# Optimization experiments

Measured on AMD Instinct MI355X. Metric: run time of the kernel, lower is better.

The kernel has to match this reference:

```python
import jax, jax.numpy as jnp
import numpy as np

DROPOUT_P = 0.2


def setup_inputs() -> dict:
    key = jax.random.key(0)
    kq, kk, kv = jax.random.split(key, 3)
    B, Sq, Sk, D, Dv = 4, 4096, 4096, 64, 64
    return {
        "query": jax.random.normal(kq, (B, Sq, D), dtype=jnp.float32),
        "key": jax.random.normal(kk, (B, Sk, D), dtype=jnp.float32),
        "value": jax.random.normal(kv, (B, Sk, Dv), dtype=jnp.float32),
        "inv_scale_factor": 8,
    }


def reference(query, key, value, inv_scale_factor):
    # qk = Q K^T / inv_scale_factor  -> [B, Sq, Sk]
    scaled_qk = jnp.einsum("bqd,bkd->bqk", query, key) / inv_scale_factor
    probs = jax.nn.softmax(scaled_qk, axis=-1)
    # dropout (train mode, p=0.2) with a fixed key for determinism
    keep = jax.random.bernoulli(jax.random.key(42), 1.0 - DROPOUT_P, probs.shape)
    probs = jnp.where(keep, probs / (1.0 - DROPOUT_P), 0.0)
    # [B, Sq, Sk] @ [B, Sk, Dv] -> [B, Sq, Dv]
    return jnp.einsum("bqk,bkv->bqv", probs, value)
```

## Files before the change

### kernel.cpp

```cpp
#include <hip/hip_runtime.h>
#include <stdint.h>

#define S_LEN 4096
#define D_DIM 64
#define KBLK  64
#define QBLK  64
#define NBATCH 4
#define ROWSTRIDE 66

typedef __attribute__((ext_vector_type(8))) short bf16x8;
typedef __attribute__((ext_vector_type(4))) float f32x4;

#define LOG2E 1.4426950408889634f

__device__ __forceinline__ uint32_t pk_bf16(float lo, float hi) {
    uint32_t r;
    asm("v_cvt_pk_bf16_f32 %0, %1, %2" : "=v"(r) : "v"(lo), "v"(hi));
    return r;
}
__device__ __forceinline__ uint32_t rotl32(uint32_t x, int n) {
    return __builtin_amdgcn_alignbit(x, x, 32 - n);
}

__device__ __forceinline__ uint32_t threefry_xor(uint32_t idx) {
    const uint32_t k0 = 0u, k1 = 42u;
    const uint32_t k2 = 0x1BD11BDAu ^ k0 ^ k1;
    uint32_t x0 = k0;
    uint32_t x1 = idx + k1;
#define TFR(r) { x0 += x1; x1 = rotl32(x1, (r)); x1 ^= x0; }
    TFR(13) TFR(15) TFR(26) TFR(6)
    x0 += k1; x1 += k2 + 1u;
    TFR(17) TFR(29) TFR(16) TFR(24)
    x0 += k2; x1 += k0 + 2u;
    TFR(13) TFR(15) TFR(26) TFR(6)
    x0 += k0; x1 += k1 + 3u;
    TFR(17) TFR(29) TFR(16) TFR(24)
    x0 += k1; x1 += k2 + 4u;
    TFR(13) TFR(15) TFR(26) TFR(6)
    x0 += k2; x1 += k0 + 5u;
#undef TFR
    return x0 ^ x1;
}

#define KEEP_THRESH 0xCCCCCE00u

__device__ __forceinline__ int swzV(int d) {
    return (((d & 7) ^ ((d >> 2) & 7)) << 4);
}

template <bool DIRECT>
__global__ __launch_bounds__(256, 2)
void attn_fwd_kernel(const float* __restrict__ Qp,
                     const float* __restrict__ Kp,
                     const float* __restrict__ Vp,
                     const int* __restrict__ isf,
                     float* __restrict__ outp,
                     int seg_tiles) {
    const int tid  = threadIdx.x;
    const int w    = tid >> 6;
    const int lane = tid & 63;
    const int g    = lane >> 4;
    const int lq   = lane & 15;
    const int b    = blockIdx.y;
    const int qwave = blockIdx.x * QBLK + w * 16;

    __shared__ __align__(16) unsigned char smem[16384];
    unsigned char* Kl = smem;
    unsigned char* Vt = smem + 8192;
    unsigned char* Pl = smem + w * 2048;

    float fv;
    {
        int iv = isf[0];
        if (iv >= 1 && iv <= (1 << 20)) fv = (float)iv;
        else {
            float f = __int_as_float(iv);
            fv = (f > 1.0e-3f && f < 1.0e6f) ? f : 8.0f;
        }
    }
    const float sc = LOG2E / fv;

    bf16x8 qf[2];
    {
        const float* qp = Qp + (size_t)(b * S_LEN + qwave + lq) * D_DIM + 8 * g;
        #pragma unroll
        for (int h = 0; h < 2; ++h) {
            float4 a = *(const float4*)(qp + 32 * h);
            float4 c = *(const float4*)(qp + 32 * h + 4);
            uint32_t w0 = pk_bf16(a.x * sc, a.y * sc);
            uint32_t w1 = pk_bf16(a.z * sc, a.w * sc);
            uint32_t w2 = pk_bf16(c.x * sc, c.y * sc);
            uint32_t w3 = pk_bf16(c.z * sc, c.w * sc);
            bf16x8 f;
            f[0] = (short)(w0 & 0xFFFF); f[1] = (short)(w0 >> 16);
            f[2] = (short)(w1 & 0xFFFF); f[3] = (short)(w1 >> 16);
            f[4] = (short)(w2 & 0xFFFF); f[5] = (short)(w2 >> 16);
            f[6] = (short)(w3 & 0xFFFF); f[7] = (short)(w3 >> 16);
            qf[h] = f;
        }
    }

    f32x4 acc[4];
    #pragma unroll
    for (int nt = 0; nt < 4; ++nt) { acc[nt][0]=0.f; acc[nt][1]=0.f; acc[nt][2]=0.f; acc[nt][3]=0.f; }
    float lrun = 0.0f;

    const float* Kb = Kp + (size_t)b * S_LEN * D_DIM;
    const float* Vb = Vp + (size_t)b * S_LEN * D_DIM;

    const int kt0 = blockIdx.z * seg_tiles;
    for (int kt = kt0; kt < kt0 + seg_tiles; ++kt) {
        const int kbase = kt * KBLK;
        __syncthreads();

        #pragma unroll
        for (int i = 0; i < 4; ++i) {
            int p4 = i * 256 + tid;
            int r  = p4 >> 4, c4 = p4 & 15;
            float4 v = *(const float4*)(Kb + (size_t)(kbase + r) * D_DIM + c4 * 4);
            uint2 wv; wv.x = pk_bf16(v.x, v.y); wv.y = pk_bf16(v.z, v.w);
            *(uint2*)(Kl + ((r * 128 + c4 * 8) ^ ((r & 7) << 4))) = wv;
        }
        #pragma unroll
        for (int i = 0; i < 2; ++i) {
            int pp = i * 256 + tid;
            int kp = pp >> 4, d4 = (pp & 15) * 4;
            const float* vp = Vb + (size_t)(kbase + 2 * kp) * D_DIM + d4;
            float4 a = *(const float4*)vp;
            float4 c = *(const float4*)(vp + D_DIM);
            *(uint32_t*)(Vt + (((d4 + 0) * 128 + kp * 4) ^ swzV(d4 + 0))) = pk_bf16(a.x, c.x);
            *(uint32_t*)(Vt + (((d4 + 1) * 128 + kp * 4) ^ swzV(d4 + 1))) = pk_bf16(a.y, c.y);
            *(uint32_t*)(Vt + (((d4 + 2) * 128 + kp * 4) ^ swzV(d4 + 2))) = pk_bf16(a.z, c.z);
            *(uint32_t*)(Vt + (((d4 + 3) * 128 + kp * 4) ^ swzV(d4 + 3))) = pk_bf16(a.w, c.w);
        }
        __syncthreads();

        f32x4 s[4];
        #pragma unroll
        for (int mt = 0; mt < 4; ++mt) { s[mt][0]=0.f; s[mt][1]=0.f; s[mt][2]=0.f; s[mt][3]=0.f; }
        #pragma unroll
        for (int h = 0; h < 2; ++h) {
            #pragma unroll
            for (int mt = 0; mt < 4; ++mt) {
                int r = 16 * mt + lq;
                bf16x8 kf = *(const bf16x8*)(Kl + ((r * 128 + (4 * h + g) * 16) ^ ((r & 7) << 4)));
                s[mt] = __builtin_amdgcn_mfma_f32_16x16x32_bf16(kf, qf[h], s[mt], 0, 0, 0);
            }
        }
        __syncthreads();

        float pvv[4][4];
        float tsum = 0.f;
        #pragma unroll
        for (int mt = 0; mt < 4; ++mt)
            #pragma unroll
            for (int r = 0; r < 4; ++r) {
                float e = __builtin_amdgcn_exp2f(s[mt][r]);
                pvv[mt][r] = e; tsum += e;
            }
        tsum += __shfl_xor(tsum, 16);
        tsum += __shfl_xor(tsum, 32);
        lrun += tsum;

        const uint32_t base2 = ((uint32_t)b << 24) + ((uint32_t)(qwave + lq) << 12)
                             + (uint32_t)kbase + 4u * (uint32_t)g;
        uint32_t bits[16];
        #pragma unroll
        for (int mt = 0; mt < 4; ++mt)
            #pragma unroll
            for (int r = 0; r < 4; ++r)
                bits[4 * mt + r] = threefry_xor(base2 + (uint32_t)(16 * mt + r));

        #pragma unroll
        for (int mt = 0; mt < 4; ++mt) {
            float pd0 = (bits[4 * mt + 0] < KEEP_THRESH) ? pvv[mt][0] : 0.0f;
            float pd1 = (bits[4 * mt + 1] < KEEP_THRESH) ? pvv[mt][1] : 0.0f;
            float pd2 = (bits[4 * mt + 2] < KEEP_THRESH) ? pvv[mt][2] : 0.0f;
            float pd3 = (bits[4 * mt + 3] < KEEP_THRESH) ? pvv[mt][3] : 0.0f;
            uint2 pw; pw.x = pk_bf16(pd0, pd1); pw.y = pk_bf16(pd2, pd3);
            *(uint2*)(Pl + ((lq * 128 + (16 * mt + 4 * g) * 2) ^ ((lq & 7) << 4))) = pw;
        }

        asm volatile("" ::: "memory");

        #pragma unroll
        for (int kk = 0; kk < 2; ++kk) {
            bf16x8 pf = *(const bf16x8*)(Pl + ((lq * 128 + kk * 64 + g * 16) ^ ((lq & 7) << 4)));
            #pragma unroll
            for (int nt = 0; nt < 4; ++nt) {
                int d = lq + 16 * nt;
                bf16x8 vf = *(const bf16x8*)(Vt + ((d * 128 + kk * 64 + g * 16) ^ swzV(d)));
                acc[nt] = __builtin_amdgcn_mfma_f32_16x16x32_bf16(pf, vf, acc[nt], 0, 0, 0);
            }
        }
    }

    if (DIRECT) {
        float l0 = __shfl(lrun, 4 * g + 0);
        float l1 = __shfl(lrun, 4 * g + 1);
        float l2 = __shfl(lrun, 4 * g + 2);
        float l3 = __shfl(lrun, 4 * g + 3);
        float inv0 = 1.0f / (l0 * 0.8f);
        float inv1 = 1.0f / (l1 * 0.8f);
        float inv2 = 1.0f / (l2 * 0.8f);
        float inv3 = 1.0f / (l3 * 0.8f);
        float* Ob = outp + (size_t)b * S_LEN * D_DIM;
        #pragma unroll
        for (int nt = 0; nt < 4; ++nt) {
            int d = lq + 16 * nt;
            Ob[(size_t)(qwave + 4 * g + 0) * D_DIM + d] = acc[nt][0] * inv0;
            Ob[(size_t)(qwave + 4 * g + 1) * D_DIM + d] = acc[nt][1] * inv1;
            Ob[(size_t)(qwave + 4 * g + 2) * D_DIM + d] = acc[nt][2] * inv2;
            Ob[(size_t)(qwave + 4 * g + 3) * D_DIM + d] = acc[nt][3] * inv3;
        }
    } else {
        float* seg = outp + (size_t)blockIdx.z * NBATCH * S_LEN * ROWSTRIDE;
        size_t row0 = (size_t)b * S_LEN + qwave;
        if (g == 0) {
            float* p = seg + (row0 + lq) * ROWSTRIDE;
            p[0] = 0.0f; p[1] = lrun;
        }
        #pragma unroll
        for (int nt = 0; nt < 4; ++nt) {
            int d = lq + 16 * nt;
            seg[(row0 + 4 * g + 0) * ROWSTRIDE + 2 + d] = acc[nt][0];
            seg[(row0 + 4 * g + 1) * ROWSTRIDE + 2 + d] = acc[nt][1];
            seg[(row0 + 4 * g + 2) * ROWSTRIDE + 2 + d] = acc[nt][2];
            seg[(row0 + 4 * g + 3) * ROWSTRIDE + 2 + d] = acc[nt][3];
        }
    }
}

__global__ void combine_kernel(const float* __restrict__ ws, float* __restrict__ Op, int NS) {
    const int tid = threadIdx.x;
    const size_t row = (size_t)blockIdx.x * 4 + (tid >> 6);
    const int d = tid & 63;
    const size_t SEGF = (size_t)NBATCH * S_LEN * ROWSTRIDE;
    const size_t roff = row * ROWSTRIDE;

    float l = 0.f, o = 0.f;
    for (int s = 0; s < NS; ++s) {
        const float* p = ws + s * SEGF + roff;
        l += p[1];
        o += p[2 + d];
    }
    Op[row * D_DIM + d] = o / (l * 0.8f);
}

extern "C" void kernel_launch(void* const* d_in, const int* in_sizes, int n_in,
                              void* d_out, int out_size, void* d_ws, size_t ws_size,
                              hipStream_t stream) {
    const float* Q = (const float*)d_in[0];
    const float* K = (const float*)d_in[1];
    const float* V = (const float*)d_in[2];
    const int* isf = (const int*)d_in[3];
    float* O = (float*)d_out;

    const size_t SEGB = (size_t)NBATCH * S_LEN * ROWSTRIDE * sizeof(float);
    int NS = 8;
    while (NS > 1 && ws_size < (size_t)NS * SEGB) NS >>= 1;

    if (NS >= 2) {
        dim3 grid1(S_LEN / QBLK, NBATCH, NS);
        attn_fwd_kernel<false><<<grid1, dim3(256), 0, stream>>>(
            Q, K, V, isf, (float*)d_ws, (S_LEN / KBLK) / NS);
        dim3 grid2((NBATCH * S_LEN) / 4);
        combine_kernel<<<grid2, dim3(256), 0, stream>>>((const float*)d_ws, O, NS);
    } else {
        dim3 grid(S_LEN / QBLK, NBATCH, 1);
        attn_fwd_kernel<true><<<grid, dim3(256), 0, stream>>>(
            Q, K, V, isf, O, S_LEN / KBLK);
    }
}
```

Before: 151.8 us.

## Pre-convert K/V to swizzled bf16 and load tiles via global_load_lds

```diff
diff --git a/kernel.cpp b/kernel.cpp
--- a/kernel.cpp
+++ b/kernel.cpp
@@ -7,6 +7,7 @@
 #define QBLK  64
 #define NBATCH 4
 #define ROWSTRIDE 66
+#define PRE_BYTES (2u * 2097152u)
 
 typedef __attribute__((ext_vector_type(8))) short bf16x8;
 typedef __attribute__((ext_vector_type(4))) float f32x4;
@@ -48,14 +49,44 @@
     return (((d & 7) ^ ((d >> 2) & 7)) << 4);
 }
 
+__device__ __forceinline__ void gll16(const void* g, void* l) {
+    __builtin_amdgcn_global_load_lds(
+        (const __attribute__((address_space(1))) uint32_t*)g,
+        (__attribute__((address_space(3))) uint32_t*)l, 16, 0, 0);
+}
+
+__global__ void prep_kernel(const float* __restrict__ Kp,
+                            const float* __restrict__ Vp,
+                            uint32_t* __restrict__ Kpre,
+                            uint32_t* __restrict__ Vpre) {
+    int gid = blockIdx.x * 256 + threadIdx.x;
+    int chunk = gid >> 11;
+    int o = (gid & 2047) << 2;
+    int b = chunk >> 6;
+    int kbase = (chunk & 63) << 6;
+    {
+        int r = o >> 7;
+        int inner = (o & 127) ^ ((r & 7) << 4);
+        int c0 = inner >> 1;
+        const float* src = Kp + ((size_t)b * S_LEN + kbase + r) * D_DIM + c0;
+        Kpre[gid] = pk_bf16(src[0], src[1]);
+    }
+    {
+        int d = o >> 7;
+        int inner = (o & 127) ^ swzV(d);
+        int kp = inner >> 2;
+        const float* src = Vp + ((size_t)b * S_LEN + kbase + 2 * kp) * D_DIM + d;
+        Vpre[gid] = pk_bf16(src[0], src[D_DIM]);
+    }
+}
+
 template <bool DIRECT>
-__global__ __launch_bounds__(256, 2)
-void attn_fwd_kernel(const float* __restrict__ Qp,
-                     const float* __restrict__ Kp,
-                     const float* __restrict__ Vp,
-                     const int* __restrict__ isf,
-                     float* __restrict__ outp,
-                     int seg_tiles) {
+__global__ void attn_fwd_kernel(const float* __restrict__ Qp,
+                                const unsigned char* __restrict__ Kpre,
+                                const unsigned char* __restrict__ Vpre,
+                                const int* __restrict__ isf,
+                                float* __restrict__ outp,
+                                int seg_tiles) {
     const int tid  = threadIdx.x;
     const int w    = tid >> 6;
     const int lane = tid & 63;
@@ -64,10 +95,10 @@
     const int b    = blockIdx.y;
     const int qwave = blockIdx.x * QBLK + w * 16;
 
-    __shared__ __align__(16) unsigned char smem[16384];
+    __shared__ __align__(16) unsigned char smem[24576];
     unsigned char* Kl = smem;
     unsigned char* Vt = smem + 8192;
-    unsigned char* Pl = smem + w * 2048;
+    unsigned char* Pl = smem + 16384 + w * 2048;
 
     float fv;
     {
@@ -105,33 +136,20 @@
     for (int nt = 0; nt < 4; ++nt) { acc[nt][0]=0.f; acc[nt][1]=0.f; acc[nt][2]=0.f; acc[nt][3]=0.f; }
     float lrun = 0.0f;
 
-    const float* Kb = Kp + (size_t)b * S_LEN * D_DIM;
-    const float* Vb = Vp + (size_t)b * S_LEN * D_DIM;
-
     const int kt0 = blockIdx.z * seg_tiles;
     for (int kt = kt0; kt < kt0 + seg_tiles; ++kt) {
         const int kbase = kt * KBLK;
         __syncthreads();
 
-        #pragma unroll
-        for (int i = 0; i < 4; ++i) {
-            int p4 = i * 256 + tid;
-            int r  = p4 >> 4, c4 = p4 & 15;
-            float4 v = *(const float4*)(Kb + (size_t)(kbase + r) * D_DIM + c4 * 4);
-            uint2 wv; wv.x = pk_bf16(v.x, v.y); wv.y = pk_bf16(v.z, v.w);
-            *(uint2*)(Kl + ((r * 128 + c4 * 8) ^ ((r & 7) << 4))) = wv;
-        }
-        #pragma unroll
-        for (int i = 0; i < 2; ++i) {
-            int pp = i * 256 + tid;
-            int kp = pp >> 4, d4 = (pp & 15) * 4;
-            const float* vp = Vb + (size_t)(kbase + 2 * kp) * D_DIM + d4;
-            float4 a = *(const float4*)vp;
-            float4 c = *(const float4*)(vp + D_DIM);
-            *(uint32_t*)(Vt + (((d4 + 0) * 128 + kp * 4) ^ swzV(d4 + 0))) = pk_bf16(a.x, c.x);
-            *(uint32_t*)(Vt + (((d4 + 1) * 128 + kp * 4) ^ swzV(d4 + 1))) = pk_bf16(a.y, c.y);
-            *(uint32_t*)(Vt + (((d4 + 2) * 128 + kp * 4) ^ swzV(d4 + 2))) = pk_bf16(a.z, c.z);
-            *(uint32_t*)(Vt + (((d4 + 3) * 128 + kp * 4) ^ swzV(d4 + 3))) = pk_bf16(a.w, c.w);
+        {
+            const unsigned char* kc = Kpre + ((size_t)(b * 64 + kt) << 13);
+            const unsigned char* vc = Vpre + ((size_t)(b * 64 + kt) << 13);
+            int co = w * 2048 + lane * 16;
+            #pragma unroll
+            for (int j = 0; j < 2; ++j) {
+                gll16(kc + co + j * 1024, Kl + w * 2048 + j * 1024);
+                gll16(vc + co + j * 1024, Vt + w * 2048 + j * 1024);
+            }
         }
         __syncthreads();
 
@@ -147,7 +165,6 @@
                 s[mt] = __builtin_amdgcn_mfma_f32_16x16x32_bf16(kf, qf[h], s[mt], 0, 0, 0);
             }
         }
-        __syncthreads();
 
         float pvv[4][4];
         float tsum = 0.f;
@@ -256,19 +273,25 @@
     const int* isf = (const int*)d_in[3];
     float* O = (float*)d_out;
 
+    unsigned char* Kpre = (unsigned char*)d_ws;
+    unsigned char* Vpre = Kpre + 2097152;
+    float* segs = (float*)((unsigned char*)d_ws + PRE_BYTES);
+
+    prep_kernel<<<dim3(2048), dim3(256), 0, stream>>>(K, V, (uint32_t*)Kpre, (uint32_t*)Vpre);
+
     const size_t SEGB = (size_t)NBATCH * S_LEN * ROWSTRIDE * sizeof(float);
     int NS = 8;
-    while (NS > 1 && ws_size < (size_t)NS * SEGB) NS >>= 1;
-
-    if (NS >= 2) {
+    while (NS > 1 && ws_size < PRE_BYTES + (size_t)NS * SEGB) NS >>= 1;
+
+    if (NS >= 2 && ws_size >= PRE_BYTES + 2 * SEGB) {
         dim3 grid1(S_LEN / QBLK, NBATCH, NS);
         attn_fwd_kernel<false><<<grid1, dim3(256), 0, stream>>>(
-            Q, K, V, isf, (float*)d_ws, (S_LEN / KBLK) / NS);
+            Q, Kpre, Vpre, isf, segs, (S_LEN / KBLK) / NS);
         dim3 grid2((NBATCH * S_LEN) / 4);
-        combine_kernel<<<grid2, dim3(256), 0, stream>>>((const float*)d_ws, O, NS);
+        combine_kernel<<<grid2, dim3(256), 0, stream>>>(segs, O, NS);
     } else {
         dim3 grid(S_LEN / QBLK, NBATCH, 1);
         attn_fwd_kernel<true><<<grid, dim3(256), 0, stream>>>(
-            Q, K, V, isf, O, S_LEN / KBLK);
-    }
-}
+            Q, Kpre, Vpre, isf, O, S_LEN / KBLK);
+    }
+}
```

Result: no change. 150.7 us (-0.7%).
